# Kernel tuning notes

Hardware: AMD Instinct MI355X
Metric: run time of the kernel (lower is better)

Reference implementation:

```python
import jax, jax.numpy as jnp
import numpy as np

DATA_SIZE = 16
WIDTH = 128
BATCH = 4096
T0 = 0.0
DT = 0.1
T1 = 1.0
N_STEPS = 10  # round((T1 - T0) / DT), ConstantStepSize + dt0=0.1


def setup_inputs() -> dict:
    key = jax.random.key(0)
    ks = jax.random.split(key, 7)

    def init(k, shape):
        fan_in = shape[-1]
        return jax.random.normal(k, shape, jnp.float32) / np.float32(np.sqrt(fan_in))

    return {
        "y": jax.random.normal(ks[0], (BATCH, DATA_SIZE), jnp.float32),
        "W1": init(ks[1], (WIDTH, DATA_SIZE + 1)),
        "b1": jax.random.normal(ks[2], (WIDTH,), jnp.float32) * 0.01,
        "W2": init(ks[3], (WIDTH, WIDTH)),
        "b2": jax.random.normal(ks[4], (WIDTH,), jnp.float32) * 0.01,
        "W3": init(ks[5], (DATA_SIZE, WIDTH)),
        "b3": jax.random.normal(ks[6], (DATA_SIZE,), jnp.float32) * 0.01,
    }


def reference(y, W1, b1, W2, b2, W3, b3):
    """ContinuousNormalizingFlow.transform_and_log_det with exact_logp=True,
    ReversibleHeun solver, ConstantStepSize, vmapped over a batch of samples.
    Returns (transformed_y [B, d], delta_log_likelihood [B])."""
    d = y.shape[-1]

    def drift(t, yv):  # yv: [d] -> [d]   (MLPFunc.__call__)
        x = jnp.concatenate([yv, t[None]])  # [d+1]
        h = jax.nn.silu(W1 @ x + b1)
        h = jax.nn.silu(W2 @ h + b2)
        return W3 @ h + b3

    def drift_and_trace(t, yv):  # exact_logp_wrapper per sample
        f, vjp_fn = jax.vjp(lambda z: drift(t, z), yv)
        (dfdy,) = jax.vmap(vjp_fn)(jnp.eye(d, dtype=yv.dtype))  # [d, d]
        return f, jnp.trace(dfdy)

    vf = jax.vmap(drift_and_trace, in_axes=(None, 0))  # -> ([B, d], [B])

    dt = jnp.float32(DT)
    t0 = jnp.float32(T0)
    l0 = jnp.zeros(y.shape[0], y.dtype)

    # ReversibleHeun: auxiliary state yhat starts at y0, vf evaluated once at t0.
    fy0, fl0 = vf(t0, y)
    state = (y, l0, y, l0, fy0, fl0)

    def step(state, i):
        yc, lc, yh, lh, fy, fl = state
        t1 = t0 + (i.astype(jnp.float32) + 1.0) * dt
        yh1 = 2.0 * yc - yh + dt * fy
        lh1 = 2.0 * lc - lh + dt * fl
        fy1, fl1 = vf(t1, yh1)
        y1 = yc + 0.5 * dt * (fy + fy1)
        l1 = lc + 0.5 * dt * (fl + fl1)
        return (y1, l1, yh1, lh1, fy1, fl1), None

    state, _ = jax.lax.scan(step, state, jnp.arange(N_STEPS))
    return state[0], state[1]
```

## Files before the change

kernel.cpp:

```cpp
#include <hip/hip_runtime.h>
#include <stdint.h>

typedef _Float16 f16x8 __attribute__((ext_vector_type(8)));
typedef float f32x4 __attribute__((ext_vector_type(4)));

#define MFMA16(a, b, c) __builtin_amdgcn_mfma_f32_16x16x32_f16(a, b, c, 0, 0, 0)

static __device__ __forceinline__ uint32_t pkh(float a, float b) {
    union { _Float16 h[2]; uint32_t u; } v;
    v.h[0] = (_Float16)a; v.h[1] = (_Float16)b;
    return v.u;
}

__global__ void cnf_prep(const float* __restrict__ W1, const float* __restrict__ W2,
                         const float* __restrict__ W3, _Float16* __restrict__ Gh) {
    int idx = blockIdx.x * 256 + threadIdx.x;
    int i = idx >> 7, k = idx & 127;
    float m = 0.f;
#pragma unroll
    for (int mm = 0; mm < 16; ++mm) m += W1[i * 17 + mm] * W3[mm * 128 + k];
    Gh[idx] = (_Float16)(m * W2[k * 128 + i]);
}

__launch_bounds__(256, 1)
__global__ void cnf_main(const float* __restrict__ y,
                         const float* __restrict__ W1, const float* __restrict__ b1,
                         const float* __restrict__ W2, const float* __restrict__ b2,
                         const float* __restrict__ W3, const float* __restrict__ b3,
                         const _Float16* __restrict__ Gh, float* __restrict__ out) {
    __shared__ _Float16 H1[128 * 16];
    __shared__ _Float16 H2[128 * 16];
    __shared__ _Float16 S2[128 * 16];
    __shared__ float PS[4 * 16];

    const int tid = threadIdx.x;
    const int w   = tid >> 6;
    const int l   = tid & 63;
    const int col = l & 15;
    const int g4  = l >> 4;
    const int sbase = blockIdx.x * 16;

    f16x8 W1f[2], W2f[2][4], Gf[2][4], W3f[4];
    float b1r[2][4], b2r[2][4], b3r[4];
#pragma unroll
    for (int m = 0; m < 2; ++m) {
        const int row = w * 32 + m * 16 + col;
        f16x8 a;
#pragma unroll
        for (int j = 0; j < 8; ++j) {
            int k = g4 * 8 + j;
            a[j] = (_Float16)(k < 17 ? W1[row * 17 + k] : 0.f);
        }
        W1f[m] = a;
#pragma unroll
        for (int ks = 0; ks < 4; ++ks) {
            const float4* pw = (const float4*)&W2[row * 128 + ks * 32 + g4 * 8];
            float4 w0 = pw[0], w1 = pw[1];
            f16x8 aw = {(_Float16)w0.x, (_Float16)w0.y, (_Float16)w0.z, (_Float16)w0.w,
                        (_Float16)w1.x, (_Float16)w1.y, (_Float16)w1.z, (_Float16)w1.w};
            W2f[m][ks] = aw;
            Gf[m][ks]  = *(const f16x8*)&Gh[row * 128 + ks * 32 + g4 * 8];
        }
#pragma unroll
        for (int r = 0; r < 4; ++r) {
            int rr = w * 32 + m * 16 + g4 * 4 + r;
            b1r[m][r] = b1[rr];
            b2r[m][r] = b2[rr];
        }
    }
#pragma unroll
    for (int ks = 0; ks < 4; ++ks) {
        const float4* pw = (const float4*)&W3[col * 128 + ks * 32 + g4 * 8];
        float4 w0 = pw[0], w1 = pw[1];
        f16x8 a = {(_Float16)w0.x, (_Float16)w0.y, (_Float16)w0.z, (_Float16)w0.w,
                   (_Float16)w1.x, (_Float16)w1.y, (_Float16)w1.z, (_Float16)w1.w};
        W3f[ks] = a;
    }
#pragma unroll
    for (int r = 0; r < 4; ++r) b3r[r] = b3[g4 * 4 + r];

    f32x4 yc, yh, fy, xsrc;
#pragma unroll
    for (int r = 0; r < 4; ++r) {
        float v = y[(sbase + col) * 16 + g4 * 4 + r];
        yc[r] = v; yh[r] = v; xsrc[r] = v;
    }
    float plsum = 0.f;

    for (int e = 0; e <= 10; ++e) {
        const float t = 0.1f * (float)e;

        uint32_t u0 = pkh(xsrc[0], xsrc[1]);
        uint32_t u1 = pkh(xsrc[2], xsrc[3]);
        int s0 = (g4 * 32 + col) & 63;
        uint32_t xw0 = (uint32_t)__shfl((int)u0, s0);
        uint32_t xw1 = (uint32_t)__shfl((int)u1, s0);
        uint32_t xw2 = (uint32_t)__shfl((int)u0, (s0 + 16) & 63);
        uint32_t xw3 = (uint32_t)__shfl((int)u1, (s0 + 16) & 63);
        if (g4 == 2) { xw0 = pkh(t, 0.f); xw1 = 0u; xw2 = 0u; xw3 = 0u; }
        if (g4 == 3) { xw0 = 0u; xw1 = 0u; xw2 = 0u; xw3 = 0u; }
        union { uint32_t u[4]; f16x8 f; } xu;
        xu.u[0] = xw0; xu.u[1] = xw1; xu.u[2] = xw2; xu.u[3] = xw3;
        f16x8 Xf = xu.f;

        float s1v[2][4];
#pragma unroll
        for (int m = 0; m < 2; ++m) {
            f32x4 c = {b1r[m][0], b1r[m][1], b1r[m][2], b1r[m][3]};
            c = MFMA16(W1f[m], Xf, c);
            uint32_t pk0, pk1;
            {
                float z0 = c[0], z1 = c[1], z2 = c[2], z3 = c[3];
                float g0 = 1.f / (1.f + __expf(-z0)), g1 = 1.f / (1.f + __expf(-z1));
                float g2 = 1.f / (1.f + __expf(-z2)), g3 = 1.f / (1.f + __expf(-z3));
                float h0 = z0 * g0, h1 = z1 * g1, h2 = z2 * g2, h3 = z3 * g3;
                s1v[m][0] = g0 + h0 * (1.f - g0); s1v[m][1] = g1 + h1 * (1.f - g1);
                s1v[m][2] = g2 + h2 * (1.f - g2); s1v[m][3] = g3 + h3 * (1.f - g3);
                pk0 = pkh(h0, h1); pk1 = pkh(h2, h3);
            }
            int rowb = w * 32 + m * 16 + g4 * 4;
            uint32_t* p = (uint32_t*)&H1[(rowb >> 3) * 128 + col * 8 + (rowb & 7)];
            p[0] = pk0; p[1] = pk1;
        }
        __syncthreads();

        f16x8 Bf[4];
#pragma unroll
        for (int ks = 0; ks < 4; ++ks)
            Bf[ks] = *(const f16x8*)&H1[(g4 + ks * 4) * 128 + col * 8];
#pragma unroll
        for (int m = 0; m < 2; ++m) {
            f32x4 ca = {b2r[m][0], b2r[m][1], b2r[m][2], b2r[m][3]};
            f32x4 cb = {0.f, 0.f, 0.f, 0.f};
            ca = MFMA16(W2f[m][0], Bf[0], ca);
            cb = MFMA16(W2f[m][1], Bf[1], cb);
            ca = MFMA16(W2f[m][2], Bf[2], ca);
            cb = MFMA16(W2f[m][3], Bf[3], cb);
            uint32_t h0u, h1u, s0u, s1u;
            {
                float z0 = ca[0] + cb[0], z1 = ca[1] + cb[1];
                float z2 = ca[2] + cb[2], z3 = ca[3] + cb[3];
                float g0 = 1.f / (1.f + __expf(-z0)), g1 = 1.f / (1.f + __expf(-z1));
                float g2 = 1.f / (1.f + __expf(-z2)), g3 = 1.f / (1.f + __expf(-z3));
                float h0 = z0 * g0, h1 = z1 * g1, h2 = z2 * g2, h3 = z3 * g3;
                h0u = pkh(h0, h1); h1u = pkh(h2, h3);
                s0u = pkh(g0 + h0 * (1.f - g0), g1 + h1 * (1.f - g1));
                s1u = pkh(g2 + h2 * (1.f - g2), g3 + h3 * (1.f - g3));
            }
            int rowb = w * 32 + m * 16 + g4 * 4;
            int idx  = (rowb >> 3) * 128 + col * 8 + (rowb & 7);
            uint32_t* p2 = (uint32_t*)&H2[idx];
            p2[0] = h0u; p2[1] = h1u;
            uint32_t* p3 = (uint32_t*)&S2[idx];
            p3[0] = s0u; p3[1] = s1u;
        }
        __syncthreads();

        f16x8 Sf[4], Hf[4];
#pragma unroll
        for (int ks = 0; ks < 4; ++ks) {
            Sf[ks] = *(const f16x8*)&S2[(g4 + ks * 4) * 128 + col * 8];
            Hf[ks] = *(const f16x8*)&H2[(g4 + ks * 4) * 128 + col * 8];
        }
        float p = 0.f;
#pragma unroll
        for (int m = 0; m < 2; ++m) {
            f32x4 c0 = {0.f, 0.f, 0.f, 0.f}, c1 = {0.f, 0.f, 0.f, 0.f};
            c0 = MFMA16(Gf[m][0], Sf[0], c0);
            c1 = MFMA16(Gf[m][1], Sf[1], c1);
            c0 = MFMA16(Gf[m][2], Sf[2], c0);
            c1 = MFMA16(Gf[m][3], Sf[3], c1);
#pragma unroll
            for (int r = 0; r < 4; ++r) p += s1v[m][r] * (c0[r] + c1[r]);
        }
        p += __shfl_xor(p, 16);
        p += __shfl_xor(p, 32);
        plsum += ((e == 0 || e == 10) ? 0.05f : 0.1f) * p;

        f32x4 fa = {b3r[0], b3r[1], b3r[2], b3r[3]};
        f32x4 fb = {0.f, 0.f, 0.f, 0.f};
        fa = MFMA16(W3f[0], Hf[0], fa);
        fb = MFMA16(W3f[1], Hf[1], fb);
        fa = MFMA16(W3f[2], Hf[2], fa);
        fb = MFMA16(W3f[3], Hf[3], fb);

        if (e == 0) {
#pragma unroll
            for (int r = 0; r < 4; ++r) fy[r] = fa[r] + fb[r];
        } else {
#pragma unroll
            for (int r = 0; r < 4; ++r) {
                float fn = fa[r] + fb[r];
                yc[r] += 0.05f * (fy[r] + fn);
                fy[r] = fn;
            }
        }
        if (e < 10) {
#pragma unroll
            for (int r = 0; r < 4; ++r) {
                float v = 2.f * yc[r] - yh[r] + 0.1f * fy[r];
                xsrc[r] = v;
                yh[r] = v;
            }
        }
    }

    if (l < 16) PS[w * 16 + l] = plsum;
    __syncthreads();
    if (w == 0) {
#pragma unroll
        for (int r = 0; r < 4; ++r)
            out[(sbase + col) * 16 + g4 * 4 + r] = yc[r];
        if (l < 16)
            out[4096 * 16 + sbase + l] = PS[l] + PS[16 + l] + PS[32 + l] + PS[48 + l];
    }
}

extern "C" void kernel_launch(void* const* d_in, const int* in_sizes, int n_in,
                              void* d_out, int out_size, void* d_ws, size_t ws_size,
                              hipStream_t stream) {
    const float* y  = (const float*)d_in[0];
    const float* W1 = (const float*)d_in[1];
    const float* b1 = (const float*)d_in[2];
    const float* W2 = (const float*)d_in[3];
    const float* b2 = (const float*)d_in[4];
    const float* W3 = (const float*)d_in[5];
    const float* b3 = (const float*)d_in[6];
    float* out = (float*)d_out;
    _Float16* Gh = (_Float16*)d_ws;

    cnf_prep<<<64, 256, 0, stream>>>(W1, W2, W3, Gh);
    cnf_main<<<256, 256, 0, stream>>>(y, W1, b1, W2, b2, W3, b3, Gh, out);
}
```

Baseline: 30.36 us.

## Propagate state in hidden-layer-1 space, fold prep kernel into main, use 8 waves

The ODE state is reparameterized as u = W1[:, :16]·y, so each step multiplies by a precomputed M = W1·W3 instead of running the W1 and W3 layers separately. The final y is recovered once at the end through W3 applied to the time-weighted sum of h2. The separate prep kernel that built G is removed; each block now computes M and G itself. Blocks grow to 512 threads, one 16-row tile per wave. This trades a launch and per-step MFMAs for redundant per-block setup work and some numerical differences from the reformulation.

```diff
diff --git a/kernel.cpp b/kernel.cpp
--- a/kernel.cpp
+++ b/kernel.cpp
@@ -12,115 +12,130 @@
     return v.u;
 }
 
-__global__ void cnf_prep(const float* __restrict__ W1, const float* __restrict__ W2,
-                         const float* __restrict__ W3, _Float16* __restrict__ Gh) {
-    int idx = blockIdx.x * 256 + threadIdx.x;
-    int i = idx >> 7, k = idx & 127;
-    float m = 0.f;
-#pragma unroll
-    for (int mm = 0; mm < 16; ++mm) m += W1[i * 17 + mm] * W3[mm * 128 + k];
-    Gh[idx] = (_Float16)(m * W2[k * 128 + i]);
-}
-
-__launch_bounds__(256, 1)
+__launch_bounds__(512, 2)
 __global__ void cnf_main(const float* __restrict__ y,
                          const float* __restrict__ W1, const float* __restrict__ b1,
                          const float* __restrict__ W2, const float* __restrict__ b2,
                          const float* __restrict__ W3, const float* __restrict__ b3,
-                         const _Float16* __restrict__ Gh, float* __restrict__ out) {
-    __shared__ _Float16 H1[128 * 16];
-    __shared__ _Float16 H2[128 * 16];
-    __shared__ _Float16 S2[128 * 16];
-    __shared__ float PS[4 * 16];
-
-    const int tid = threadIdx.x;
-    const int w   = tid >> 6;
-    const int l   = tid & 63;
-    const int col = l & 15;
-    const int g4  = l >> 4;
+                         float* __restrict__ out) {
+    __shared__ _Float16 H1[16 * 128];
+    __shared__ _Float16 H2[16 * 128];
+    __shared__ _Float16 S2[16 * 128];
+    __shared__ float PS[8 * 16];
+
+    const int tid   = threadIdx.x;
+    const int w     = tid >> 6;
+    const int l     = tid & 63;
+    const int col   = l & 15;
+    const int g4    = l >> 4;
     const int sbase = blockIdx.x * 16;
-
-    f16x8 W1f[2], W2f[2][4], Gf[2][4], W3f[4];
-    float b1r[2][4], b2r[2][4], b3r[4];
-#pragma unroll
-    for (int m = 0; m < 2; ++m) {
-        const int row = w * 32 + m * 16 + col;
-        f16x8 a;
+    const int arow  = w * 16 + col;
+    const int crow  = w * 16 + g4 * 4;
+
+    f16x8 W2f[4], Gf[4], Mf[4];
+#pragma unroll
+    for (int ks = 0; ks < 4; ++ks) {
+        const float4* pw = (const float4*)&W2[arow * 128 + ks * 32 + g4 * 8];
+        float4 a0 = pw[0], a1 = pw[1];
+        f16x8 t = {(_Float16)a0.x, (_Float16)a0.y, (_Float16)a0.z, (_Float16)a0.w,
+                   (_Float16)a1.x, (_Float16)a1.y, (_Float16)a1.z, (_Float16)a1.w};
+        W2f[ks] = t;
+    }
+    float macc[4][8];
+#pragma unroll
+    for (int ks = 0; ks < 4; ++ks)
+#pragma unroll
+        for (int j = 0; j < 8; ++j) macc[ks][j] = 0.f;
+#pragma unroll
+    for (int m = 0; m < 16; ++m) {
+        float wv = W1[arow * 17 + m];
+#pragma unroll
+        for (int ks = 0; ks < 4; ++ks) {
+            const float4* pr = (const float4*)&W3[m * 128 + ks * 32 + g4 * 8];
+            float4 r0 = pr[0], r1 = pr[1];
+            macc[ks][0] += wv * r0.x; macc[ks][1] += wv * r0.y;
+            macc[ks][2] += wv * r0.z; macc[ks][3] += wv * r0.w;
+            macc[ks][4] += wv * r1.x; macc[ks][5] += wv * r1.y;
+            macc[ks][6] += wv * r1.z; macc[ks][7] += wv * r1.w;
+        }
+    }
+#pragma unroll
+    for (int ks = 0; ks < 4; ++ks) {
+        f16x8 mh, gh;
 #pragma unroll
         for (int j = 0; j < 8; ++j) {
-            int k = g4 * 8 + j;
-            a[j] = (_Float16)(k < 17 ? W1[row * 17 + k] : 0.f);
-        }
-        W1f[m] = a;
-#pragma unroll
-        for (int ks = 0; ks < 4; ++ks) {
-            const float4* pw = (const float4*)&W2[row * 128 + ks * 32 + g4 * 8];
-            float4 w0 = pw[0], w1 = pw[1];
-            f16x8 aw = {(_Float16)w0.x, (_Float16)w0.y, (_Float16)w0.z, (_Float16)w0.w,
-                        (_Float16)w1.x, (_Float16)w1.y, (_Float16)w1.z, (_Float16)w1.w};
-            W2f[m][ks] = aw;
-            Gf[m][ks]  = *(const f16x8*)&Gh[row * 128 + ks * 32 + g4 * 8];
-        }
-#pragma unroll
-        for (int r = 0; r < 4; ++r) {
-            int rr = w * 32 + m * 16 + g4 * 4 + r;
-            b1r[m][r] = b1[rr];
-            b2r[m][r] = b2[rr];
-        }
-    }
-#pragma unroll
-    for (int ks = 0; ks < 4; ++ks) {
-        const float4* pw = (const float4*)&W3[col * 128 + ks * 32 + g4 * 8];
-        float4 w0 = pw[0], w1 = pw[1];
-        f16x8 a = {(_Float16)w0.x, (_Float16)w0.y, (_Float16)w0.z, (_Float16)w0.w,
-                   (_Float16)w1.x, (_Float16)w1.y, (_Float16)w1.z, (_Float16)w1.w};
-        W3f[ks] = a;
-    }
-#pragma unroll
-    for (int r = 0; r < 4; ++r) b3r[r] = b3[g4 * 4 + r];
-
-    f32x4 yc, yh, fy, xsrc;
+            float mv = macc[ks][j];
+            mh[j] = (_Float16)mv;
+            gh[j] = (_Float16)(mv * W2[(ks * 32 + g4 * 8 + j) * 128 + arow]);
+        }
+        Mf[ks] = mh;
+        Gf[ks] = gh;
+    }
+
+    float b1r[4], b2r[4], w1t[4], ub3[4];
 #pragma unroll
     for (int r = 0; r < 4; ++r) {
-        float v = y[(sbase + col) * 16 + g4 * 4 + r];
-        yc[r] = v; yh[r] = v; xsrc[r] = v;
-    }
+        b1r[r] = b1[crow + r];
+        b2r[r] = b2[crow + r];
+        w1t[r] = W1[(crow + r) * 17 + 16];
+        float acc = 0.f;
+#pragma unroll
+        for (int m = 0; m < 16; ++m) acc += W1[(crow + r) * 17 + m] * b3[m];
+        ub3[r] = acc;
+    }
+
+    f32x4 uc, uh, uf = {0.f, 0.f, 0.f, 0.f}, hacc = {0.f, 0.f, 0.f, 0.f};
+    {
+        union { uint32_t u[4]; f16x8 f; } yu, wu;
+#pragma unroll
+        for (int q = 0; q < 4; ++q) { yu.u[q] = 0u; wu.u[q] = 0u; }
+        if (g4 < 2) {
+            const float4* py = (const float4*)&y[(sbase + col) * 16 + g4 * 8];
+            float4 y0 = py[0], y1 = py[1];
+            yu.u[0] = pkh(y0.x, y0.y); yu.u[1] = pkh(y0.z, y0.w);
+            yu.u[2] = pkh(y1.x, y1.y); yu.u[3] = pkh(y1.z, y1.w);
+            wu.u[0] = pkh(W1[arow * 17 + g4 * 8 + 0], W1[arow * 17 + g4 * 8 + 1]);
+            wu.u[1] = pkh(W1[arow * 17 + g4 * 8 + 2], W1[arow * 17 + g4 * 8 + 3]);
+            wu.u[2] = pkh(W1[arow * 17 + g4 * 8 + 4], W1[arow * 17 + g4 * 8 + 5]);
+            wu.u[3] = pkh(W1[arow * 17 + g4 * 8 + 6], W1[arow * 17 + g4 * 8 + 7]);
+        }
+        f32x4 z0 = {0.f, 0.f, 0.f, 0.f};
+        uc = MFMA16(wu.f, yu.f, z0);
+    }
+    uh = uc;
+
     float plsum = 0.f;
+    const int hidx = ((crow >> 3) * 16 + col) * 8 + (crow & 7);
 
     for (int e = 0; e <= 10; ++e) {
-        const float t = 0.1f * (float)e;
-
-        uint32_t u0 = pkh(xsrc[0], xsrc[1]);
-        uint32_t u1 = pkh(xsrc[2], xsrc[3]);
-        int s0 = (g4 * 32 + col) & 63;
-        uint32_t xw0 = (uint32_t)__shfl((int)u0, s0);
-        uint32_t xw1 = (uint32_t)__shfl((int)u1, s0);
-        uint32_t xw2 = (uint32_t)__shfl((int)u0, (s0 + 16) & 63);
-        uint32_t xw3 = (uint32_t)__shfl((int)u1, (s0 + 16) & 63);
-        if (g4 == 2) { xw0 = pkh(t, 0.f); xw1 = 0u; xw2 = 0u; xw3 = 0u; }
-        if (g4 == 3) { xw0 = 0u; xw1 = 0u; xw2 = 0u; xw3 = 0u; }
-        union { uint32_t u[4]; f16x8 f; } xu;
-        xu.u[0] = xw0; xu.u[1] = xw1; xu.u[2] = xw2; xu.u[3] = xw3;
-        f16x8 Xf = xu.f;
-
-        float s1v[2][4];
-#pragma unroll
-        for (int m = 0; m < 2; ++m) {
-            f32x4 c = {b1r[m][0], b1r[m][1], b1r[m][2], b1r[m][3]};
-            c = MFMA16(W1f[m], Xf, c);
-            uint32_t pk0, pk1;
-            {
-                float z0 = c[0], z1 = c[1], z2 = c[2], z3 = c[3];
-                float g0 = 1.f / (1.f + __expf(-z0)), g1 = 1.f / (1.f + __expf(-z1));
-                float g2 = 1.f / (1.f + __expf(-z2)), g3 = 1.f / (1.f + __expf(-z3));
-                float h0 = z0 * g0, h1 = z1 * g1, h2 = z2 * g2, h3 = z3 * g3;
-                s1v[m][0] = g0 + h0 * (1.f - g0); s1v[m][1] = g1 + h1 * (1.f - g1);
-                s1v[m][2] = g2 + h2 * (1.f - g2); s1v[m][3] = g3 + h3 * (1.f - g3);
-                pk0 = pkh(h0, h1); pk1 = pkh(h2, h3);
-            }
-            int rowb = w * 32 + m * 16 + g4 * 4;
-            uint32_t* p = (uint32_t*)&H1[(rowb >> 3) * 128 + col * 8 + (rowb & 7)];
-            p[0] = pk0; p[1] = pk1;
+        const float t  = 0.1f * (float)e;
+        const float wt = (e == 0 || e == 10) ? 0.05f : 0.1f;
+
+        f32x4 z1;
+        if (e == 0) {
+#pragma unroll
+            for (int r = 0; r < 4; ++r) z1[r] = uc[r] + b1r[r];
+        } else {
+#pragma unroll
+            for (int r = 0; r < 4; ++r) {
+                uh[r] = 2.f * uc[r] - uh[r] + 0.1f * uf[r];
+                z1[r] = uh[r] + t * w1t[r] + b1r[r];
+            }
+        }
+        float s1v[4];
+        {
+            float h1v[4];
+#pragma unroll
+            for (int r = 0; r < 4; ++r) {
+                float zz = z1[r];
+                float g  = 1.f / (1.f + __expf(-zz));
+                float hh = zz * g;
+                h1v[r] = hh;
+                s1v[r] = g + hh * (1.f - g);
+            }
+            uint32_t* p = (uint32_t*)&H1[hidx];
+            p[0] = pkh(h1v[0], h1v[1]);
+            p[1] = pkh(h1v[2], h1v[3]);
         }
         __syncthreads();
 
@@ -128,91 +143,101 @@
 #pragma unroll
         for (int ks = 0; ks < 4; ++ks)
             Bf[ks] = *(const f16x8*)&H1[(g4 + ks * 4) * 128 + col * 8];
-#pragma unroll
-        for (int m = 0; m < 2; ++m) {
-            f32x4 ca = {b2r[m][0], b2r[m][1], b2r[m][2], b2r[m][3]};
-            f32x4 cb = {0.f, 0.f, 0.f, 0.f};
-            ca = MFMA16(W2f[m][0], Bf[0], ca);
-            cb = MFMA16(W2f[m][1], Bf[1], cb);
-            ca = MFMA16(W2f[m][2], Bf[2], ca);
-            cb = MFMA16(W2f[m][3], Bf[3], cb);
-            uint32_t h0u, h1u, s0u, s1u;
-            {
-                float z0 = ca[0] + cb[0], z1 = ca[1] + cb[1];
-                float z2 = ca[2] + cb[2], z3 = ca[3] + cb[3];
-                float g0 = 1.f / (1.f + __expf(-z0)), g1 = 1.f / (1.f + __expf(-z1));
-                float g2 = 1.f / (1.f + __expf(-z2)), g3 = 1.f / (1.f + __expf(-z3));
-                float h0 = z0 * g0, h1 = z1 * g1, h2 = z2 * g2, h3 = z3 * g3;
-                h0u = pkh(h0, h1); h1u = pkh(h2, h3);
-                s0u = pkh(g0 + h0 * (1.f - g0), g1 + h1 * (1.f - g1));
-                s1u = pkh(g2 + h2 * (1.f - g2), g3 + h3 * (1.f - g3));
-            }
-            int rowb = w * 32 + m * 16 + g4 * 4;
-            int idx  = (rowb >> 3) * 128 + col * 8 + (rowb & 7);
-            uint32_t* p2 = (uint32_t*)&H2[idx];
-            p2[0] = h0u; p2[1] = h1u;
-            uint32_t* p3 = (uint32_t*)&S2[idx];
-            p3[0] = s0u; p3[1] = s1u;
+        f32x4 ca = {b2r[0], b2r[1], b2r[2], b2r[3]};
+        f32x4 cb = {0.f, 0.f, 0.f, 0.f};
+        ca = MFMA16(W2f[0], Bf[0], ca); cb = MFMA16(W2f[1], Bf[1], cb);
+        ca = MFMA16(W2f[2], Bf[2], ca); cb = MFMA16(W2f[3], Bf[3], cb);
+        {
+            float h2v[4], s2v[4];
+#pragma unroll
+            for (int r = 0; r < 4; ++r) {
+                float zz = ca[r] + cb[r];
+                float g  = 1.f / (1.f + __expf(-zz));
+                float hh = zz * g;
+                h2v[r] = hh;
+                s2v[r] = g + hh * (1.f - g);
+                hacc[r] += wt * hh;
+            }
+            if (e < 10) {
+                uint32_t* p = (uint32_t*)&H2[hidx];
+                p[0] = pkh(h2v[0], h2v[1]);
+                p[1] = pkh(h2v[2], h2v[3]);
+            }
+            uint32_t* p = (uint32_t*)&S2[hidx];
+            p[0] = pkh(s2v[0], s2v[1]);
+            p[1] = pkh(s2v[2], s2v[3]);
         }
         __syncthreads();
 
-        f16x8 Sf[4], Hf[4];
-#pragma unroll
-        for (int ks = 0; ks < 4; ++ks) {
+        f16x8 Sf[4];
+#pragma unroll
+        for (int ks = 0; ks < 4; ++ks)
             Sf[ks] = *(const f16x8*)&S2[(g4 + ks * 4) * 128 + col * 8];
-            Hf[ks] = *(const f16x8*)&H2[(g4 + ks * 4) * 128 + col * 8];
-        }
+        f32x4 c0 = {0.f, 0.f, 0.f, 0.f}, c1 = {0.f, 0.f, 0.f, 0.f};
+        c0 = MFMA16(Gf[0], Sf[0], c0); c1 = MFMA16(Gf[1], Sf[1], c1);
+        c0 = MFMA16(Gf[2], Sf[2], c0); c1 = MFMA16(Gf[3], Sf[3], c1);
         float p = 0.f;
 #pragma unroll
-        for (int m = 0; m < 2; ++m) {
-            f32x4 c0 = {0.f, 0.f, 0.f, 0.f}, c1 = {0.f, 0.f, 0.f, 0.f};
-            c0 = MFMA16(Gf[m][0], Sf[0], c0);
-            c1 = MFMA16(Gf[m][1], Sf[1], c1);
-            c0 = MFMA16(Gf[m][2], Sf[2], c0);
-            c1 = MFMA16(Gf[m][3], Sf[3], c1);
-#pragma unroll
-            for (int r = 0; r < 4; ++r) p += s1v[m][r] * (c0[r] + c1[r]);
-        }
+        for (int r = 0; r < 4; ++r) p += s1v[r] * (c0[r] + c1[r]);
         p += __shfl_xor(p, 16);
         p += __shfl_xor(p, 32);
-        plsum += ((e == 0 || e == 10) ? 0.05f : 0.1f) * p;
-
-        f32x4 fa = {b3r[0], b3r[1], b3r[2], b3r[3]};
-        f32x4 fb = {0.f, 0.f, 0.f, 0.f};
-        fa = MFMA16(W3f[0], Hf[0], fa);
-        fb = MFMA16(W3f[1], Hf[1], fb);
-        fa = MFMA16(W3f[2], Hf[2], fa);
-        fb = MFMA16(W3f[3], Hf[3], fb);
-
-        if (e == 0) {
-#pragma unroll
-            for (int r = 0; r < 4; ++r) fy[r] = fa[r] + fb[r];
-        } else {
-#pragma unroll
-            for (int r = 0; r < 4; ++r) {
-                float fn = fa[r] + fb[r];
-                yc[r] += 0.05f * (fy[r] + fn);
-                fy[r] = fn;
-            }
-        }
+        plsum += wt * p;
+
         if (e < 10) {
-#pragma unroll
-            for (int r = 0; r < 4; ++r) {
-                float v = 2.f * yc[r] - yh[r] + 0.1f * fy[r];
-                xsrc[r] = v;
-                yh[r] = v;
-            }
-        }
-    }
-
+            f16x8 Hf[4];
+#pragma unroll
+            for (int ks = 0; ks < 4; ++ks)
+                Hf[ks] = *(const f16x8*)&H2[(g4 + ks * 4) * 128 + col * 8];
+            f32x4 u0 = {ub3[0], ub3[1], ub3[2], ub3[3]};
+            f32x4 u1 = {0.f, 0.f, 0.f, 0.f};
+            u0 = MFMA16(Mf[0], Hf[0], u0); u1 = MFMA16(Mf[1], Hf[1], u1);
+            u0 = MFMA16(Mf[2], Hf[2], u0); u1 = MFMA16(Mf[3], Hf[3], u1);
+            if (e == 0) {
+#pragma unroll
+                for (int r = 0; r < 4; ++r) uf[r] = u0[r] + u1[r];
+            } else {
+#pragma unroll
+                for (int r = 0; r < 4; ++r) {
+                    float un = u0[r] + u1[r];
+                    uc[r] += 0.05f * (uf[r] + un);
+                    uf[r] = un;
+                }
+            }
+        }
+    }
+
+    {
+        uint32_t* p = (uint32_t*)&H2[hidx];
+        p[0] = pkh(hacc[0], hacc[1]);
+        p[1] = pkh(hacc[2], hacc[3]);
+    }
     if (l < 16) PS[w * 16 + l] = plsum;
     __syncthreads();
     if (w == 0) {
+        f16x8 Hf[4], W3w[4];
+#pragma unroll
+        for (int ks = 0; ks < 4; ++ks) {
+            Hf[ks] = *(const f16x8*)&H2[(g4 + ks * 4) * 128 + col * 8];
+            const float4* pw = (const float4*)&W3[col * 128 + ks * 32 + g4 * 8];
+            float4 a0 = pw[0], a1 = pw[1];
+            f16x8 t = {(_Float16)a0.x, (_Float16)a0.y, (_Float16)a0.z, (_Float16)a0.w,
+                       (_Float16)a1.x, (_Float16)a1.y, (_Float16)a1.z, (_Float16)a1.w};
+            W3w[ks] = t;
+        }
+        f32x4 f0 = {b3[g4 * 4 + 0], b3[g4 * 4 + 1], b3[g4 * 4 + 2], b3[g4 * 4 + 3]};
+        f32x4 f1 = {0.f, 0.f, 0.f, 0.f};
+        f0 = MFMA16(W3w[0], Hf[0], f0); f1 = MFMA16(W3w[1], Hf[1], f1);
+        f0 = MFMA16(W3w[2], Hf[2], f0); f1 = MFMA16(W3w[3], Hf[3], f1);
 #pragma unroll
         for (int r = 0; r < 4; ++r)
-            out[(sbase + col) * 16 + g4 * 4 + r] = yc[r];
-        if (l < 16)
-            out[4096 * 16 + sbase + l] = PS[l] + PS[16 + l] + PS[32 + l] + PS[48 + l];
+            out[(sbase + col) * 16 + g4 * 4 + r] =
+                y[(sbase + col) * 16 + g4 * 4 + r] + f0[r] + f1[r];
+        if (l < 16) {
+            float s = 0.f;
+#pragma unroll
+            for (int ww = 0; ww < 8; ++ww) s += PS[ww * 16 + l];
+            out[4096 * 16 + sbase + l] = s;
+        }
     }
 }
 
@@ -227,8 +252,6 @@
     const float* W3 = (const float*)d_in[5];
     const float* b3 = (const float*)d_in[6];
     float* out = (float*)d_out;
-    _Float16* Gh = (_Float16*)d_ws;
-
-    cnf_prep<<<64, 256, 0, stream>>>(W1, W2, W3, Gh);
-    cnf_main<<<256, 256, 0, stream>>>(y, W1, b1, W2, b2, W3, b3, Gh, out);
+
+    cnf_main<<<256, 512, 0, stream>>>(y, W1, b1, W2, b2, W3, b3, out);
 }
```

Measured after the change: 89.44 us. 195% more time.
